# Optimization experiments

Measured on AMD Instinct MI355X. Metric: run time of the kernel, lower is better.

The kernel has to match this reference:

```python
import jax, jax.numpy as jnp
import numpy as np

B, C, W, H = 8, 64, 256, 256


def setup_inputs() -> dict:
    key = jax.random.key(0)
    ks = jax.random.split(key, 7)
    s = lambda n: 1.0 / np.sqrt(n)
    return {
        "x": jax.random.normal(ks[0], (B, C, W, H), dtype=jnp.float32),
        "Wc": jax.random.uniform(ks[1], (C, C), jnp.float32, -s(C), s(C)),
        "bc": jax.random.uniform(ks[2], (C,), jnp.float32, -s(C), s(C)),
        "Ww": jax.random.uniform(ks[3], (W, W), jnp.float32, -s(W), s(W)),
        "bw": jax.random.uniform(ks[4], (W,), jnp.float32, -s(W), s(W)),
        "Wh": jax.random.uniform(ks[5], (H, H), jnp.float32, -s(H), s(H)),
        "bh": jax.random.uniform(ks[6], (H,), jnp.float32, -s(H), s(H)),
    }


def reference(x, Wc, bc, Ww, bw, Wh, bh):
    # SE-style gates: global avg-pool over the two non-gated dims, 1x1 conv
    # (= dense on pooled vector), sigmoid. x is (B, C, W, H).
    c = jax.nn.sigmoid(jnp.einsum("oc,bc->bo", Wc, x.mean((2, 3))) + bc)  # (B, C)
    w = jax.nn.sigmoid(jnp.einsum("ow,bw->bo", Ww, x.mean((1, 3))) + bw)  # (B, W)
    h = jax.nn.sigmoid(jnp.einsum("oh,bh->bo", Wh, x.mean((1, 2))) + bh)  # (B, H)
    # Rank-1 tensor (triple outer product) per batch, broadcast-fused:
    return c[:, :, None, None] * w[:, None, :, None] * h[:, None, None, :]
```

## Files before the change

kernel.cpp:

```cpp
#include <hip/hip_runtime.h>


#define NB 8
#define NC 64
#define NW 256
#define NH 256


__global__ __launch_bounds__(256) void pool_kernel(const float* __restrict__ x,
                                                   float* __restrict__ ws) {
    float* sum_c = ws;
    float* sum_w = ws + 512;
    float* sum_h = ws + 2560;

    int blk  = blockIdx.x;
    int bc   = blk >> 1;
    int half = blk & 1;
    int b    = bc >> 6;
    int tid  = threadIdx.x;
    int wv   = tid >> 6;
    int lane = tid & 63;

    const float4* xr = (const float4*)x + (size_t)bc * (NW * (NH / 4));
    int wbase = half * 128;

    float4 col = make_float4(0.f, 0.f, 0.f, 0.f);
    __shared__ float rowsum[4][32];
    __shared__ float cols[4][NH];
    __shared__ float wpart[4];

    for (int kb = 0; kb < 32; kb += 8) {
        float4 v[8];
        #pragma unroll
        for (int i = 0; i < 8; ++i)
            v[i] = xr[(wbase + wv + 4 * (kb + i)) * (NH / 4) + lane];
        float rs[8];
        #pragma unroll
        for (int i = 0; i < 8; ++i) {
            col.x += v[i].x; col.y += v[i].y; col.z += v[i].z; col.w += v[i].w;
            rs[i] = (v[i].x + v[i].y) + (v[i].z + v[i].w);
        }
        #pragma unroll
        for (int off = 32; off; off >>= 1) {
            #pragma unroll
            for (int i = 0; i < 8; ++i) rs[i] += __shfl_xor(rs[i], off);
        }
        #pragma unroll
        for (int i = 0; i < 8; ++i)
            if (lane == i) rowsum[wv][kb + i] = rs[i];
    }

    cols[wv][lane * 4 + 0] = col.x;
    cols[wv][lane * 4 + 1] = col.y;
    cols[wv][lane * 4 + 2] = col.z;
    cols[wv][lane * 4 + 3] = col.w;
    __syncthreads();

    float cv = cols[0][tid] + cols[1][tid] + cols[2][tid] + cols[3][tid];
    atomicAdd(&sum_h[b * NH + tid], cv);

    if (tid < 128)
        atomicAdd(&sum_w[b * NW + wbase + tid], rowsum[tid & 3][tid >> 2]);

    float t = cv;
    #pragma unroll
    for (int off = 32; off; off >>= 1) t += __shfl_xor(t, off);
    if (lane == 0) wpart[wv] = t;
    __syncthreads();
    if (tid == 0) atomicAdd(&sum_c[bc], wpart[0] + wpart[1] + wpart[2] + wpart[3]);
}

__global__ __launch_bounds__(256) void gates_kernel(const float* __restrict__ Wc, const float* __restrict__ bc_,
                                                    const float* __restrict__ Ww, const float* __restrict__ bw_,
                                                    const float* __restrict__ Wh, const float* __restrict__ bh_,
                                                    float* __restrict__ ws) {
    const float* sum_c = ws;
    const float* sum_w = ws + 512;
    const float* sum_h = ws + 2560;
    float* gate_c = ws + 4608;
    float* gate_w = ws + 5120;
    float* gate_h = ws + 7168;

    int j = blockIdx.x * 4 + (threadIdx.x >> 6);
    int lane = threadIdx.x & 63;

    float acc = 0.f, bias;
    float* dst;
    if (j < 512) {
        int b = j >> 6, o = j & 63;
        acc = Wc[o * 64 + lane] * sum_c[b * 64 + lane] * (1.f / 65536.f);
        bias = bc_[o];
        dst = &gate_c[j];
    } else if (j < 2560) {
        int j2 = j - 512;
        int b = j2 >> 8, o = j2 & 255;
        const float* wr = Ww + o * 256;
        const float* sr = sum_w + b * 256;
        #pragma unroll
        for (int m = 0; m < 4; ++m) acc += wr[lane + 64 * m] * sr[lane + 64 * m];
        acc *= (1.f / 16384.f);
        bias = bw_[o];
        dst = &gate_w[j2];
    } else {
        int j2 = j - 2560;
        int b = j2 >> 8, o = j2 & 255;
        const float* wr = Wh + o * 256;
        const float* sr = sum_h + b * 256;
        #pragma unroll
        for (int m = 0; m < 4; ++m) acc += wr[lane + 64 * m] * sr[lane + 64 * m];
        acc *= (1.f / 16384.f);
        bias = bh_[o];
        dst = &gate_h[j2];
    }
    #pragma unroll
    for (int off = 32; off; off >>= 1) acc += __shfl_xor(acc, off);
    if (lane == 0) *dst = 1.f / (1.f + expf(-(acc + bias)));
}

__global__ __launch_bounds__(256) void out_kernel(const float* __restrict__ ws,
                                                  float4* __restrict__ out) {
    const float* gate_c = ws + 4608;
    const float* gate_w = ws + 5120;
    const float4* gate_h4 = (const float4*)(ws + 7168);

    const size_t N4 = (size_t)NB * NC * NW * (NH / 4);
    size_t stride = (size_t)gridDim.x * blockDim.x;
    for (size_t i = (size_t)blockIdx.x * blockDim.x + threadIdx.x; i < N4; i += stride) {
        int h4 = (int)(i & 63);
        size_t row = i >> 6;
        int w = (int)(row & 255);
        size_t bcr = row >> 8;
        int c = (int)(bcr & 63);
        int b = (int)(bcr >> 6);
        float g = gate_c[b * 64 + c] * gate_w[b * 256 + w];
        float4 gh = gate_h4[b * 64 + h4];
        out[i] = make_float4(g * gh.x, g * gh.y, g * gh.z, g * gh.w);
    }
}

extern "C" void kernel_launch(void* const* d_in, const int* in_sizes, int n_in,
                              void* d_out, int out_size, void* d_ws, size_t ws_size,
                              hipStream_t stream) {
    const float* x   = (const float*)d_in[0];
    const float* Wc  = (const float*)d_in[1];
    const float* bc_ = (const float*)d_in[2];
    const float* Ww  = (const float*)d_in[3];
    const float* bw_ = (const float*)d_in[4];
    const float* Wh  = (const float*)d_in[5];
    const float* bh_ = (const float*)d_in[6];
    float* ws = (float*)d_ws;

    hipMemsetAsync(ws, 0, 4608 * sizeof(float), stream);

    pool_kernel<<<1024, 256, 0, stream>>>(x, ws);
    gates_kernel<<<4608 / 4, 256, 0, stream>>>(Wc, bc_, Ww, bw_, Wh, bh_, ws);
    out_kernel<<<2048, 256, 0, stream>>>(ws, (float4*)d_out);
}
```

Measured before the change: 58.57 us.

## Replace pooling atomics with per-block partials and a separate reduce kernel

The pooling kernel now writes per-block partial sums into a scratch region of the output buffer instead of issuing atomics. A new small reduce kernel sums those partials into the workspace, and the memset is removed. The load batch in pooling grows from 8 to 16 rows, and the output kernel uses nontemporal vector stores. This trades atomic contention and the memset for an extra launch and some partial-buffer traffic.

```diff
diff --git a/kernel.cpp b/kernel.cpp
--- a/kernel.cpp
+++ b/kernel.cpp
@@ -6,17 +6,18 @@
 #define NW 256
 #define NH 256
 
+typedef float f4v __attribute__((ext_vector_type(4)));
+
 
 __global__ __launch_bounds__(256) void pool_kernel(const float* __restrict__ x,
-                                                   float* __restrict__ ws) {
-    float* sum_c = ws;
-    float* sum_w = ws + 512;
-    float* sum_h = ws + 2560;
+                                                   float* __restrict__ ps) {
+    float* part_c = ps;
+    float* part_w = ps + 1024;
+    float* part_h = ps + 132096;
 
     int blk  = blockIdx.x;
     int bc   = blk >> 1;
     int half = blk & 1;
-    int b    = bc >> 6;
     int tid  = threadIdx.x;
     int wv   = tid >> 6;
     int lane = tid & 63;
@@ -29,24 +30,24 @@
     __shared__ float cols[4][NH];
     __shared__ float wpart[4];
 
-    for (int kb = 0; kb < 32; kb += 8) {
-        float4 v[8];
+    for (int kb = 0; kb < 32; kb += 16) {
+        float4 v[16];
         #pragma unroll
-        for (int i = 0; i < 8; ++i)
+        for (int i = 0; i < 16; ++i)
             v[i] = xr[(wbase + wv + 4 * (kb + i)) * (NH / 4) + lane];
-        float rs[8];
+        float rs[16];
         #pragma unroll
-        for (int i = 0; i < 8; ++i) {
+        for (int i = 0; i < 16; ++i) {
             col.x += v[i].x; col.y += v[i].y; col.z += v[i].z; col.w += v[i].w;
             rs[i] = (v[i].x + v[i].y) + (v[i].z + v[i].w);
         }
         #pragma unroll
         for (int off = 32; off; off >>= 1) {
             #pragma unroll
-            for (int i = 0; i < 8; ++i) rs[i] += __shfl_xor(rs[i], off);
+            for (int i = 0; i < 16; ++i) rs[i] += __shfl_xor(rs[i], off);
         }
         #pragma unroll
-        for (int i = 0; i < 8; ++i)
+        for (int i = 0; i < 16; ++i)
             if (lane == i) rowsum[wv][kb + i] = rs[i];
     }
 
@@ -57,17 +58,43 @@
     __syncthreads();
 
     float cv = cols[0][tid] + cols[1][tid] + cols[2][tid] + cols[3][tid];
-    atomicAdd(&sum_h[b * NH + tid], cv);
+    part_h[(size_t)blk * 256 + tid] = cv;
 
     if (tid < 128)
-        atomicAdd(&sum_w[b * NW + wbase + tid], rowsum[tid & 3][tid >> 2]);
+        part_w[(size_t)bc * 256 + wbase + tid] = rowsum[tid & 3][tid >> 2];
 
     float t = cv;
     #pragma unroll
     for (int off = 32; off; off >>= 1) t += __shfl_xor(t, off);
     if (lane == 0) wpart[wv] = t;
     __syncthreads();
-    if (tid == 0) atomicAdd(&sum_c[bc], wpart[0] + wpart[1] + wpart[2] + wpart[3]);
+    if (tid == 0) part_c[blk] = wpart[0] + wpart[1] + wpart[2] + wpart[3];
+}
+
+__global__ __launch_bounds__(256) void reduce_kernel(const float* __restrict__ ps,
+                                                     float* __restrict__ ws) {
+    const float* part_c = ps;
+    const float* part_w = ps + 1024;
+    const float* part_h = ps + 132096;
+    int t = threadIdx.x, blk = blockIdx.x;
+
+    if (blk < 8) {
+        const float* p = part_h + (size_t)blk * 128 * 256 + t;
+        float s = 0.f;
+        #pragma unroll 8
+        for (int j = 0; j < 128; ++j) s += p[j * 256];
+        ws[2560 + blk * 256 + t] = s;
+    } else if (blk < 16) {
+        int b = blk - 8;
+        const float* p = part_w + (size_t)b * 64 * 256 + t;
+        float s = 0.f;
+        #pragma unroll 8
+        for (int c = 0; c < 64; ++c) s += p[c * 256];
+        ws[512 + b * 256 + t] = s;
+    } else {
+        ws[t]       = part_c[2 * t]         + part_c[2 * t + 1];
+        ws[256 + t] = part_c[2 * (256 + t)] + part_c[2 * (256 + t) + 1];
+    }
 }
 
 __global__ __launch_bounds__(256) void gates_kernel(const float* __restrict__ Wc, const float* __restrict__ bc_,
@@ -118,7 +145,7 @@
 }
 
 __global__ __launch_bounds__(256) void out_kernel(const float* __restrict__ ws,
-                                                  float4* __restrict__ out) {
+                                                  float* __restrict__ out) {
     const float* gate_c = ws + 4608;
     const float* gate_w = ws + 5120;
     const float4* gate_h4 = (const float4*)(ws + 7168);
@@ -134,7 +161,8 @@
         int b = (int)(bcr >> 6);
         float g = gate_c[b * 64 + c] * gate_w[b * 256 + w];
         float4 gh = gate_h4[b * 64 + h4];
-        out[i] = make_float4(g * gh.x, g * gh.y, g * gh.z, g * gh.w);
+        f4v val = {g * gh.x, g * gh.y, g * gh.z, g * gh.w};
+        __builtin_nontemporal_store(val, (f4v*)(out + 4 * i));
     }
 }
 
@@ -149,10 +177,10 @@
     const float* Wh  = (const float*)d_in[5];
     const float* bh_ = (const float*)d_in[6];
     float* ws = (float*)d_ws;
+    float* ps = (float*)d_out;
 
-    hipMemsetAsync(ws, 0, 4608 * sizeof(float), stream);
-
-    pool_kernel<<<1024, 256, 0, stream>>>(x, ws);
+    pool_kernel<<<1024, 256, 0, stream>>>(x, ps);
+    reduce_kernel<<<17, 256, 0, stream>>>(ps, ws);
     gates_kernel<<<4608 / 4, 256, 0, stream>>>(Wc, bc_, Ww, bw_, Wh, bh_, ws);
-    out_kernel<<<2048, 256, 0, stream>>>(ws, (float4*)d_out);
+    out_kernel<<<2048, 256, 0, stream>>>(ws, (float*)d_out);
 }
```

New measurement: 58.54 us. About the same (-0.1%).

## Replace atomic pooling with partial-sum buffers and restructure gates and output kernels

Applied to the files above, without the earlier changes.

The pool kernel now writes per-block partial sums into the output buffer, used as scratch, instead of issuing atomics, which also removes the memset. The gates kernel becomes one block per batch that reduces the partials in shared memory and computes all three gate GEMVs per thread. The output kernel writes a fixed tile per block with nontemporal stores and keeps the W gates in registers. The risks are an 8-block gates kernel with a long serial reduction over 256 partials, and reliance on the output buffer being large enough to hold the scratch.

```diff
diff --git a/kernel.cpp b/kernel.cpp
--- a/kernel.cpp
+++ b/kernel.cpp
@@ -6,34 +6,35 @@
 #define NW 256
 #define NH 256
 
+typedef float f4v __attribute__((ext_vector_type(4)));
+
 
 __global__ __launch_bounds__(256) void pool_kernel(const float* __restrict__ x,
-                                                   float* __restrict__ ws) {
-    float* sum_c = ws;
-    float* sum_w = ws + 512;
-    float* sum_h = ws + 2560;
-
-    int blk  = blockIdx.x;
-    int bc   = blk >> 1;
-    int half = blk & 1;
-    int b    = bc >> 6;
+                                                   float* __restrict__ ps) {
+    float* part_c = ps;
+    float* part_w = ps + 2048;
+    float* part_h = ps + 133120;
+
+    int k    = blockIdx.x;
+    int bc   = k >> 2;
+    int q    = k & 3;
     int tid  = threadIdx.x;
     int wv   = tid >> 6;
     int lane = tid & 63;
+    int wbase = q * 64;
 
     const float4* xr = (const float4*)x + (size_t)bc * (NW * (NH / 4));
-    int wbase = half * 128;
 
     float4 col = make_float4(0.f, 0.f, 0.f, 0.f);
-    __shared__ float rowsum[4][32];
+    __shared__ float rowsum[4][16];
     __shared__ float cols[4][NH];
     __shared__ float wpart[4];
 
-    for (int kb = 0; kb < 32; kb += 8) {
+    for (int jb = 0; jb < 16; jb += 8) {
         float4 v[8];
         #pragma unroll
         for (int i = 0; i < 8; ++i)
-            v[i] = xr[(wbase + wv + 4 * (kb + i)) * (NH / 4) + lane];
+            v[i] = xr[(wbase + wv + 4 * (jb + i)) * (NH / 4) + lane];
         float rs[8];
         #pragma unroll
         for (int i = 0; i < 8; ++i) {
@@ -47,7 +48,7 @@
         }
         #pragma unroll
         for (int i = 0; i < 8; ++i)
-            if (lane == i) rowsum[wv][kb + i] = rs[i];
+            if (lane == i) rowsum[wv][jb + i] = rs[i];
     }
 
     cols[wv][lane * 4 + 0] = col.x;
@@ -57,84 +58,132 @@
     __syncthreads();
 
     float cv = cols[0][tid] + cols[1][tid] + cols[2][tid] + cols[3][tid];
-    atomicAdd(&sum_h[b * NH + tid], cv);
-
-    if (tid < 128)
-        atomicAdd(&sum_w[b * NW + wbase + tid], rowsum[tid & 3][tid >> 2]);
+    part_h[(size_t)k * 256 + tid] = cv;
+
+    if (tid < 64)
+        part_w[(size_t)bc * 256 + wbase + tid] = rowsum[tid & 3][tid >> 2];
 
     float t = cv;
     #pragma unroll
     for (int off = 32; off; off >>= 1) t += __shfl_xor(t, off);
     if (lane == 0) wpart[wv] = t;
     __syncthreads();
-    if (tid == 0) atomicAdd(&sum_c[bc], wpart[0] + wpart[1] + wpart[2] + wpart[3]);
-}
-
-__global__ __launch_bounds__(256) void gates_kernel(const float* __restrict__ Wc, const float* __restrict__ bc_,
+    if (tid == 0) part_c[k] = wpart[0] + wpart[1] + wpart[2] + wpart[3];
+}
+
+__global__ __launch_bounds__(256) void gates_kernel(const float* __restrict__ ps,
+                                                    const float* __restrict__ Wc, const float* __restrict__ bc_,
                                                     const float* __restrict__ Ww, const float* __restrict__ bw_,
                                                     const float* __restrict__ Wh, const float* __restrict__ bh_,
                                                     float* __restrict__ ws) {
-    const float* sum_c = ws;
-    const float* sum_w = ws + 512;
-    const float* sum_h = ws + 2560;
+    const float* part_c = ps;
+    const float* part_w = ps + 2048;
+    const float* part_h = ps + 133120;
     float* gate_c = ws + 4608;
     float* gate_w = ws + 5120;
     float* gate_h = ws + 7168;
 
-    int j = blockIdx.x * 4 + (threadIdx.x >> 6);
-    int lane = threadIdx.x & 63;
-
-    float acc = 0.f, bias;
-    float* dst;
-    if (j < 512) {
-        int b = j >> 6, o = j & 63;
-        acc = Wc[o * 64 + lane] * sum_c[b * 64 + lane] * (1.f / 65536.f);
-        bias = bc_[o];
-        dst = &gate_c[j];
-    } else if (j < 2560) {
-        int j2 = j - 512;
-        int b = j2 >> 8, o = j2 & 255;
-        const float* wr = Ww + o * 256;
-        const float* sr = sum_w + b * 256;
-        #pragma unroll
-        for (int m = 0; m < 4; ++m) acc += wr[lane + 64 * m] * sr[lane + 64 * m];
-        acc *= (1.f / 16384.f);
-        bias = bw_[o];
-        dst = &gate_w[j2];
-    } else {
-        int j2 = j - 2560;
-        int b = j2 >> 8, o = j2 & 255;
-        const float* wr = Wh + o * 256;
-        const float* sr = sum_h + b * 256;
-        #pragma unroll
-        for (int m = 0; m < 4; ++m) acc += wr[lane + 64 * m] * sr[lane + 64 * m];
-        acc *= (1.f / 16384.f);
-        bias = bh_[o];
-        dst = &gate_h[j2];
-    }
-    #pragma unroll
-    for (int off = 32; off; off >>= 1) acc += __shfl_xor(acc, off);
-    if (lane == 0) *dst = 1.f / (1.f + expf(-(acc + bias)));
+    int b = blockIdx.x, t = threadIdx.x;
+    __shared__ float s_c[64], s_w[256], s_h[256];
+
+    {
+        const float* p = part_h + (size_t)b * 256 * 256 + t;
+        float s = 0.f;
+        for (int jb = 0; jb < 256; jb += 16) {
+            float v[16];
+            #pragma unroll
+            for (int i = 0; i < 16; ++i) v[i] = p[(jb + i) * 256];
+            float s0 = 0.f, s1 = 0.f;
+            #pragma unroll
+            for (int i = 0; i < 16; i += 2) { s0 += v[i]; s1 += v[i + 1]; }
+            s += s0 + s1;
+        }
+        s_h[t] = s;
+    }
+    {
+        const float* p = part_w + (size_t)b * 64 * 256 + t;
+        float s = 0.f;
+        for (int jb = 0; jb < 64; jb += 16) {
+            float v[16];
+            #pragma unroll
+            for (int i = 0; i < 16; ++i) v[i] = p[(jb + i) * 256];
+            float s0 = 0.f, s1 = 0.f;
+            #pragma unroll
+            for (int i = 0; i < 16; i += 2) { s0 += v[i]; s1 += v[i + 1]; }
+            s += s0 + s1;
+        }
+        s_w[t] = s;
+    }
+    if (t < 64) {
+        const float* p = part_c + (size_t)(b * 64 + t) * 4;
+        s_c[t] = (p[0] + p[1]) + (p[2] + p[3]);
+    }
+    __syncthreads();
+
+    const float4* sw4 = (const float4*)s_w;
+    const float4* sh4 = (const float4*)s_h;
+    const float4* sc4 = (const float4*)s_c;
+
+    {
+        const float4* wr = (const float4*)Ww + t * 64;
+        float acc = 0.f;
+        #pragma unroll 8
+        for (int j = 0; j < 64; ++j) {
+            float4 a = wr[j], s = sw4[j];
+            acc += a.x * s.x + a.y * s.y + a.z * s.z + a.w * s.w;
+        }
+        gate_w[b * 256 + t] = 1.f / (1.f + expf(-(acc * (1.f / 16384.f) + bw_[t])));
+    }
+    {
+        const float4* wr = (const float4*)Wh + t * 64;
+        float acc = 0.f;
+        #pragma unroll 8
+        for (int j = 0; j < 64; ++j) {
+            float4 a = wr[j], s = sh4[j];
+            acc += a.x * s.x + a.y * s.y + a.z * s.z + a.w * s.w;
+        }
+        gate_h[b * 256 + t] = 1.f / (1.f + expf(-(acc * (1.f / 16384.f) + bh_[t])));
+    }
+    if (t < 64) {
+        const float4* wr = (const float4*)Wc + t * 16;
+        float acc = 0.f;
+        #pragma unroll 8
+        for (int j = 0; j < 16; ++j) {
+            float4 a = wr[j], s = sc4[j];
+            acc += a.x * s.x + a.y * s.y + a.z * s.z + a.w * s.w;
+        }
+        gate_c[b * 64 + t] = 1.f / (1.f + expf(-(acc * (1.f / 65536.f) + bc_[t])));
+    }
 }
 
 __global__ __launch_bounds__(256) void out_kernel(const float* __restrict__ ws,
-                                                  float4* __restrict__ out) {
+                                                  float* __restrict__ out) {
     const float* gate_c = ws + 4608;
     const float* gate_w = ws + 5120;
     const float4* gate_h4 = (const float4*)(ws + 7168);
 
-    const size_t N4 = (size_t)NB * NC * NW * (NH / 4);
-    size_t stride = (size_t)gridDim.x * blockDim.x;
-    for (size_t i = (size_t)blockIdx.x * blockDim.x + threadIdx.x; i < N4; i += stride) {
-        int h4 = (int)(i & 63);
-        size_t row = i >> 6;
-        int w = (int)(row & 255);
-        size_t bcr = row >> 8;
-        int c = (int)(bcr & 63);
-        int b = (int)(bcr >> 6);
-        float g = gate_c[b * 64 + c] * gate_w[b * 256 + w];
-        float4 gh = gate_h4[b * 64 + h4];
-        out[i] = make_float4(g * gh.x, g * gh.y, g * gh.z, g * gh.w);
+    int k  = blockIdx.x;
+    int bc = k >> 2;
+    int q  = k & 3;
+    int b  = bc >> 6;
+    int t  = threadIdx.x;
+    int h4 = t & 63;
+    int wv = t >> 6;
+
+    float gc = gate_c[bc];
+    float4 gh = gate_h4[b * 64 + h4];
+
+    float gw[16];
+    #pragma unroll
+    for (int kk = 0; kk < 16; ++kk)
+        gw[kk] = gate_w[b * 256 + q * 64 + wv + 4 * kk];
+
+    float4* dst = (float4*)out + (size_t)bc * 16384 + q * 4096 + t;
+    #pragma unroll
+    for (int kk = 0; kk < 16; ++kk) {
+        float g = gc * gw[kk];
+        f4v val = {g * gh.x, g * gh.y, g * gh.z, g * gh.w};
+        __builtin_nontemporal_store(val, (f4v*)(dst + 256 * kk));
     }
 }
 
@@ -149,10 +198,9 @@
     const float* Wh  = (const float*)d_in[5];
     const float* bh_ = (const float*)d_in[6];
     float* ws = (float*)d_ws;
-
-    hipMemsetAsync(ws, 0, 4608 * sizeof(float), stream);
-
-    pool_kernel<<<1024, 256, 0, stream>>>(x, ws);
-    gates_kernel<<<4608 / 4, 256, 0, stream>>>(Wc, bc_, Ww, bw_, Wh, bh_, ws);
-    out_kernel<<<2048, 256, 0, stream>>>(ws, (float4*)d_out);
-}
+    float* ps = (float*)d_out;
+
+    pool_kernel<<<2048, 256, 0, stream>>>(x, ps);
+    gates_kernel<<<NB, 256, 0, stream>>>(ps, Wc, bc_, Ww, bw_, Wh, bh_, ws);
+    out_kernel<<<2048, 256, 0, stream>>>(ws, (float*)d_out);
+}
```

Measured after the change: 74.60 us. 27.4% more time.
